# Optimization experiments

Hardware: AMD Instinct MI355X
Metric: run time of the kernel (lower is better)

Reference implementation:

```python
import jax, jax.numpy as jnp
import numpy as np

B, M, D = 16, 16, 512          # m (tokens per sample) must equal num_experts
N = 16                          # num_experts
H = (D + D) * 2 // 3            # hidden_dim = 682
OUT = 512


def setup_inputs() -> dict:
    key = jax.random.key(0)
    ks = jax.random.split(key, 8)
    s = lambda k, shape, fan: jax.random.normal(k, shape, jnp.float32) / np.sqrt(fan)
    return {
        "x":    jax.random.normal(ks[0], (B, M, D), jnp.float32),
        "phi":  jax.random.normal(ks[1], (D, N, H), jnp.float32),
        "W1":   s(ks[2], (N, D, H), D),
        "b1":   s(ks[3], (N, H), D),
        "W2":   s(ks[4], (N, H, D), H),
        "b2":   s(ks[5], (N, D), H),
        "Wout": s(ks[6], (N * D, OUT), N * D),
        "bout": s(ks[7], (OUT,), N * D),
    }


def reference(x, phi, W1, b1, W2, b2, Wout, bout):
    # dispatch/combine logits: [b, m, n, p]
    logits = jnp.einsum('bmd,dnp->bmnp', x, phi)
    Dw = jax.nn.softmax(logits, axis=1)                       # dispatch weights over tokens m
    Cw = jax.nn.softmax(jax.nn.softmax(logits, axis=2), axis=3)  # (softmax of softmax, faithful)
    Xs = jnp.einsum('bmd,bmnp->bnpd', x, Dw)                  # expert slot inputs [b,n,p,d]
    # batched per-expert MLP (grouped GEMM over expert axis n)
    hmid = jax.nn.relu(jnp.einsum('bnpd,ndh->bnph', Xs, W1) + b1[None, :, None, :])
    Ys = jnp.einsum('bnph,nhd->bnpd', hmid, W2) + b2[None, :, None, :]
    Y = jnp.einsum('bnpd,bmnp->bmd', Ys, Cw)                  # combine -> [b, m, d]
    flat = Y.reshape(Y.shape[0], -1)                          # [b, m*d] == [b, n*d]
    return flat @ Wout + bout
```

## Files before the change

kernel.cpp:

```cpp
#include <hip/hip_runtime.h>
#include <hip/hip_bf16.h>
#include <math.h>

typedef unsigned int   u32;
typedef unsigned short u16;
typedef __bf16 bf16;
typedef bf16  bf16x8  __attribute__((ext_vector_type(8)));
typedef float f32x4   __attribute__((ext_vector_type(4)));
typedef float f32x16  __attribute__((ext_vector_type(16)));

#define BBATCH 16
#define MTOK   16
#define NEXP   16
#define DDIM   512
#define HDIM   682
#define HPAD   704
#define NHCOL  (NEXP*HDIM)
#define NHPCOL (NEXP*HPAD)
#define BM     (BBATCH*MTOK)

__device__ __forceinline__ u16 f2bf(float f) {
    u32 u = __builtin_bit_cast(u32, f);
    u += 0x7fffu + ((u >> 16) & 1u);
    return (u16)(u >> 16);
}
__device__ __forceinline__ float bf2f(u16 h) {
    u32 u = ((u32)h) << 16;
    return __builtin_bit_cast(float, u);
}
__device__ __forceinline__ u32 pk2bf(float a, float b) {
    __hip_bfloat162 t = __float22bfloat162_rn(float2{a, b});
    u32 r;
    __builtin_memcpy(&r, &t, 4);
    return r;
}

__global__ __launch_bounds__(256) void k_prep(
    const float* __restrict__ x, const float* __restrict__ b2,
    const float* __restrict__ bout,
    u16* __restrict__ xh, u16* __restrict__ xl,
    float* __restrict__ Y, float* __restrict__ out, u16* __restrict__ DwT) {
    const int bid = blockIdx.x, tid = threadIdx.x;
    if (bid < 128) {
        int i = (bid * 256 + tid) * 4;
        float4 v = *(const float4*)&x[i];
        float a[4] = {v.x, v.y, v.z, v.w};
        u16 hh[4], ll[4];
        #pragma unroll
        for (int j = 0; j < 4; ++j) {
            hh[j] = f2bf(a[j]);
            ll[j] = f2bf(a[j] - bf2f(hh[j]));
        }
        *(uint2*)&xh[i] = make_uint2((u32)hh[0] | ((u32)hh[1] << 16), (u32)hh[2] | ((u32)hh[3] << 16));
        *(uint2*)&xl[i] = make_uint2((u32)ll[0] | ((u32)ll[1] << 16), (u32)ll[2] | ((u32)ll[3] << 16));
    } else if (bid < 640) {
        int idx = (bid - 128) * 256 + tid;
        int d = idx & 511;
        float s = 0.f;
        #pragma unroll
        for (int nn = 0; nn < 16; ++nn) s += b2[nn * 512 + d];
        Y[idx] = s;
    } else if (bid < 672) {
        int idx = (bid - 640) * 256 + tid;
        out[idx] = bout[idx & 511];
    } else {
        int g = (bid - 672) * 256 + tid;
        int bn = g / 88, off = g - bn * 88;
        *(uint2*)(DwT + (size_t)(bn * HPAD + HDIM) * 16 + off * 4) = make_uint2(0u, 0u);
    }
}

__global__ __launch_bounds__(256) void k_lgemm(
    const u16* __restrict__ xh, const u16* __restrict__ xl,
    const float* __restrict__ phi, float* __restrict__ C,
    u16* __restrict__ DwT) {
    __shared__ u16 AH[128 * 40], AL[128 * 40], BH[64 * 40], BL[64 * 40];
    __shared__ float F[32 * 68];
    const int ct = blockIdx.x, rt = blockIdx.y;
    const int tid = threadIdx.x;
    const int wv = tid >> 6, lane = tid & 63, quad = lane >> 4, l15 = lane & 15;
    f32x4 acc[2][4] = {};
    for (int kb = 0; kb < 512; kb += 32) {
        {
            int rr = tid >> 2, kg = (tid & 3) * 8;
            #pragma unroll
            for (int rp = 0; rp < 2; ++rp) {
                int r = rp * 64 + rr;
                size_t ao = (size_t)(rt * 128 + r) * 512 + kb + kg;
                *(uint4*)&AH[r * 40 + kg] = *(const uint4*)(xh + ao);
                *(uint4*)&AL[r * 40 + kg] = *(const uint4*)(xl + ao);
            }
        }
        {
            int dl = tid >> 3, cg = (tid & 7) * 8;
            int c0 = ct * 64 + cg;
            const float* src = phi + (size_t)(kb + dl) * NHCOL + c0;
            float v[8];
            if (c0 + 8 <= NHCOL) {
                *(float4*)&v[0] = *(const float4*)&src[0];
                *(float4*)&v[4] = *(const float4*)&src[4];
            } else {
                #pragma unroll
                for (int i = 0; i < 8; ++i) v[i] = (c0 + i < NHCOL) ? src[i] : 0.f;
            }
            #pragma unroll
            for (int i = 0; i < 8; ++i) F[dl * 68 + cg + i] = v[i];
        }
        __syncthreads();
        {
            int cc = tid & 63, q = tid >> 6;
            u16 th[8], tl[8];
            #pragma unroll
            for (int i = 0; i < 8; ++i) {
                float v = F[(q * 8 + i) * 68 + cc];
                th[i] = f2bf(v);
                tl[i] = f2bf(v - bf2f(th[i]));
            }
            *(uint4*)&BH[cc * 40 + q * 8] = *(uint4*)&th[0];
            *(uint4*)&BL[cc * 40 + q * 8] = *(uint4*)&tl[0];
        }
        __syncthreads();
        bf16x8 ah[2], al[2];
        #pragma unroll
        for (int i = 0; i < 2; ++i) {
            ah[i] = *(const bf16x8*)&AH[(wv * 32 + i * 16 + l15) * 40 + quad * 8];
            al[i] = *(const bf16x8*)&AL[(wv * 32 + i * 16 + l15) * 40 + quad * 8];
        }
        #pragma unroll
        for (int j = 0; j < 4; ++j) {
            bf16x8 bh = *(const bf16x8*)&BH[(j * 16 + l15) * 40 + quad * 8];
            bf16x8 bl = *(const bf16x8*)&BL[(j * 16 + l15) * 40 + quad * 8];
            #pragma unroll
            for (int i = 0; i < 2; ++i) {
                acc[i][j] = __builtin_amdgcn_mfma_f32_16x16x32_bf16(ah[i], bh, acc[i][j], 0, 0, 0);
                acc[i][j] = __builtin_amdgcn_mfma_f32_16x16x32_bf16(ah[i], bl, acc[i][j], 0, 0, 0);
                acc[i][j] = __builtin_amdgcn_mfma_f32_16x16x32_bf16(al[i], bh, acc[i][j], 0, 0, 0);
            }
        }
        __syncthreads();
    }
    #pragma unroll
    for (int i = 0; i < 2; ++i) {
        const int b  = rt * 8 + wv * 2 + i;
        const int r0 = rt * 128 + wv * 32 + i * 16 + quad * 4;
        #pragma unroll
        for (int j = 0; j < 4; ++j) {
            const int col = ct * 64 + j * 16 + l15;
            float a0 = acc[i][j][0], a1 = acc[i][j][1], a2 = acc[i][j][2], a3 = acc[i][j][3];
            if (col < NHCOL) {
                C[(size_t)(r0 + 0) * NHCOL + col] = a0;
                C[(size_t)(r0 + 1) * NHCOL + col] = a1;
                C[(size_t)(r0 + 2) * NHCOL + col] = a2;
                C[(size_t)(r0 + 3) * NHCOL + col] = a3;
            }
            float mx = fmaxf(fmaxf(a0, a1), fmaxf(a2, a3));
            mx = fmaxf(mx, __shfl_xor(mx, 16));
            mx = fmaxf(mx, __shfl_xor(mx, 32));
            float e0 = expf(a0 - mx), e1 = expf(a1 - mx);
            float e2 = expf(a2 - mx), e3 = expf(a3 - mx);
            float s = e0 + e1 + e2 + e3;
            s += __shfl_xor(s, 16);
            s += __shfl_xor(s, 32);
            float inv = 1.f / s;
            if (col < NHCOL) {
                int n = col / HDIM;
                int p = col - n * HDIM;
                u16* dst = DwT + ((size_t)((b * 16 + n) * HPAD + p)) * 16 + quad * 4;
                *(uint2*)dst = make_uint2(pk2bf(e0 * inv, e1 * inv), pk2bf(e2 * inv, e3 * inv));
            }
        }
    }
}

__global__ __launch_bounds__(256) void k_t1cw(
    const u16* __restrict__ A, const float* __restrict__ W1,
    u16* __restrict__ T1b,
    const float* __restrict__ L, u16* __restrict__ CwB) {
    __shared__ __align__(16) char smem[NHCOL * 4];
    const int bid = blockIdx.x, tid = threadIdx.x;
    if (bid < 176) {
        u16*   As = (u16*)smem;
        u16*   Bs = (u16*)(smem + 20480);
        float* F  = (float*)(smem + 25600);
        const int ct = bid;
        const int wv = tid >> 6, lane = tid & 63, quad = lane >> 4, l15 = lane & 15;
        const int n = ct / 11, h0 = (ct % 11) * 64;
        f32x4 acc[4][4] = {};
        for (int kb = 0; kb < 512; kb += 32) {
            {
                int rr = tid >> 2, kg = (tid & 3) * 8;
                #pragma unroll
                for (int rp = 0; rp < 4; ++rp) {
                    int r = rp * 64 + rr;
                    *(uint4*)&As[r * 40 + kg] = *(const uint4*)(A + (size_t)r * 512 + kb + kg);
                }
            }
            {
                int dl = tid >> 3, cg = (tid & 7) * 8;
                int h = h0 + cg;
                const float* wr = W1 + ((size_t)n * 512 + kb + dl) * HDIM + h;
                float v[8];
                if (h + 8 <= HDIM) {
                    #pragma unroll
                    for (int i = 0; i < 4; ++i) {
                        float2 t = *(const float2*)&wr[i * 2];
                        v[i * 2] = t.x; v[i * 2 + 1] = t.y;
                    }
                } else {
                    #pragma unroll
                    for (int i = 0; i < 8; ++i) v[i] = (h + i < HDIM) ? wr[i] : 0.f;
                }
                #pragma unroll
                for (int i = 0; i < 8; ++i) F[dl * 68 + cg + i] = v[i];
            }
            __syncthreads();
            {
                int cc = tid & 63, q = tid >> 6;
                u16 tv[8];
                #pragma unroll
                for (int i = 0; i < 8; ++i) tv[i] = f2bf(F[(q * 8 + i) * 68 + cc]);
                *(uint4*)&Bs[cc * 40 + q * 8] = *(uint4*)&tv[0];
            }
            __syncthreads();
            bf16x8 af[4], bfr[4];
            #pragma unroll
            for (int i = 0; i < 4; ++i)
                af[i] = *(const bf16x8*)&As[(wv * 64 + i * 16 + l15) * 40 + quad * 8];
            #pragma unroll
            for (int j = 0; j < 4; ++j)
                bfr[j] = *(const bf16x8*)&Bs[(j * 16 + l15) * 40 + quad * 8];
            #pragma unroll
            for (int i = 0; i < 4; ++i)
                #pragma unroll
                for (int j = 0; j < 4; ++j)
                    acc[i][j] = __builtin_amdgcn_mfma_f32_16x16x32_bf16(af[i], bfr[j], acc[i][j], 0, 0, 0);
            __syncthreads();
        }
        #pragma unroll
        for (int i = 0; i < 4; ++i)
            #pragma unroll
            for (int j = 0; j < 4; ++j) {
                int col = ct * 64 + j * 16 + l15;
                int r0  = wv * 64 + i * 16 + quad * 4;
                #pragma unroll
                for (int r = 0; r < 4; ++r)
                    T1b[(size_t)(r0 + r) * NHPCOL + col] = f2bf(acc[i][j][r]);
            }
    } else {
        float* row = (float*)smem;
        const int j = bid - 176;
        const int m = j & 15, b = j >> 4;
        const float* Lrow = L + (size_t)(b * 16 + m) * NHCOL;
        for (int i = tid; i < NHCOL; i += 256) row[i] = Lrow[i];
        __syncthreads();
        for (int p = tid; p < HDIM; p += 256) {
            float v[16];
            float mx = -1e30f;
            #pragma unroll
            for (int n = 0; n < 16; ++n) { v[n] = row[n * HDIM + p]; mx = fmaxf(mx, v[n]); }
            float s = 0.f;
            #pragma unroll
            for (int n = 0; n < 16; ++n) { v[n] = expf(v[n] - mx); s += v[n]; }
            float inv = 1.f / s;
            #pragma unroll
            for (int n = 0; n < 16; ++n) row[n * HDIM + p] = expf(v[n] * inv);
        }
        __syncthreads();
        const int wv = tid >> 6, lane = tid & 63;
        for (int nn = 0; nn < 4; ++nn) {
            int n = wv * 4 + nn;
            float s = 0.f;
            for (int p = lane; p < HDIM; p += 64) s += row[n * HDIM + p];
            #pragma unroll
            for (int off = 32; off > 0; off >>= 1) s += __shfl_xor(s, off);
            float inv = 1.f / s;
            u16* dst = CwB + (size_t)(((b * 16 + n) * 16 + m)) * HPAD;
            for (int p = lane; p < HDIM; p += 64) dst[p] = f2bf(row[n * HDIM + p] * inv);
            if (lane < HPAD - HDIM) dst[HDIM + lane] = 0;
        }
    }
}

__global__ __launch_bounds__(256) void k_mid(
    const u16* __restrict__ T1b, const u16* __restrict__ DwT,
    const u16* __restrict__ CwB, const float* __restrict__ b1,
    u16* __restrict__ Gb) {
    __shared__ u16 T1T[128 * 24];
    __shared__ u16 hmidT[128 * 64];
    const int ht = blockIdx.x, n = blockIdx.y, b = blockIdx.z;
    const int tid = threadIdx.x;
    const int wv = tid >> 6, lane = tid & 63;
    const int quad = lane >> 4, l15 = lane & 15;
    const int l31 = lane & 31, half = lane >> 5;
    const int h0 = ht * 128;
    const int b16n = b * 16 + n;

    {
        int m = tid & 15, hh0 = (tid >> 4) * 8;
        u16 v[8];
        if (h0 + hh0 + 8 <= HPAD) {
            *(uint4*)v = *(const uint4*)(T1b + (size_t)(b * 16 + m) * NHPCOL + n * HPAD + h0 + hh0);
        } else {
            #pragma unroll
            for (int i = 0; i < 8; ++i) v[i] = 0;
        }
        #pragma unroll
        for (int i = 0; i < 8; ++i) T1T[(hh0 + i) * 24 + m] = v[i];
    }
    __syncthreads();

    const int hrow = wv * 32 + l31;
    bf16x8 bt1 = *(const bf16x8*)&T1T[hrow * 24 + half * 8];
    int hg1 = h0 + hrow;
    float biasf = (hg1 < HDIM) ? b1[n * HDIM + hg1] : 0.f;
    f32x16 cbias;
    #pragma unroll
    for (int i = 0; i < 16; ++i) cbias[i] = biasf;

    const u16* dwbase = DwT + (size_t)(b16n * HPAD) * 16;
    const u16* cwrow  = CwB + (size_t)(b16n * 16 + l15) * HPAD;

    f32x4 acc[2] = {};
    const int hsw = hrow & 7;
    for (int c = 0; c < 11; ++c) {
        const int p0 = c * 64;
        #pragma unroll
        for (int pt = 0; pt < 2; ++pt) {
            bf16x8 adw = *(const bf16x8*)(dwbase + (size_t)(p0 + pt * 32 + l31) * 16 + half * 8);
            f32x16 hm = __builtin_amdgcn_mfma_f32_32x32x16_bf16(adw, bt1, cbias, 0, 0, 0);
            #pragma unroll
            for (int g = 0; g < 4; ++g) {
                float v0 = fmaxf(hm[g * 4 + 0], 0.f);
                float v1 = fmaxf(hm[g * 4 + 1], 0.f);
                float v2 = fmaxf(hm[g * 4 + 2], 0.f);
                float v3 = fmaxf(hm[g * 4 + 3], 0.f);
                uint2 pk = make_uint2(pk2bf(v0, v1), pk2bf(v2, v3));
                int gran = (pt * 4 + g) ^ hsw;
                *(uint2*)&hmidT[hrow * 64 + gran * 8 + half * 4] = pk;
            }
        }
        #pragma unroll
        for (int s = 0; s < 2; ++s) {
            bf16x8 acw = *(const bf16x8*)(cwrow + p0 + s * 32 + quad * 8);
            #pragma unroll
            for (int hj = 0; hj < 2; ++hj) {
                int hr = wv * 32 + hj * 16 + l15;
                int gr = (s * 4 + quad) ^ (hr & 7);
                bf16x8 bh = *(const bf16x8*)&hmidT[hr * 64 + gr * 8];
                acc[hj] = __builtin_amdgcn_mfma_f32_16x16x32_bf16(acw, bh, acc[hj], 0, 0, 0);
            }
        }
    }
    #pragma unroll
    for (int hj = 0; hj < 2; ++hj) {
        int h = h0 + wv * 32 + hj * 16 + l15;
        if (h < HPAD) {
            #pragma unroll
            for (int r = 0; r < 4; ++r) {
                int m = quad * 4 + r;
                Gb[(size_t)(b * 16 + m) * NHPCOL + n * HPAD + h] = f2bf(acc[hj][r]);
            }
        }
    }
}

__global__ __launch_bounds__(256) void k_ygemm(
    const u16* __restrict__ G, const float* __restrict__ W2, float* __restrict__ Y) {
    __shared__ u16 AsL[64 * 40];
    __shared__ u16 BsL[128 * 40];
    __shared__ float F[32 * 132];
    const int ct = blockIdx.x, rt = blockIdx.y, nz = blockIdx.z;
    const int n = nz >> 1, kb0 = (nz & 1) * 352;
    const int tid = threadIdx.x;
    const int wv = tid >> 6, lane = tid & 63, quad = lane >> 4, l15 = lane & 15;
    const int m0 = rt * 64, d0 = ct * 128;
    f32x4 acc[4][2] = {};
    for (int kb = kb0; kb < kb0 + 352; kb += 32) {
        {
            int am = tid >> 2, akg = (tid & 3) * 8;
            *(uint4*)&AsL[am * 40 + akg] =
                *(const uint4*)(G + (size_t)(m0 + am) * NHPCOL + n * HPAD + kb + akg);
        }
        {
            int hl = tid >> 3, cg = (tid & 7) * 16;
            int h = kb + hl;
            float v[16];
            if (h < HDIM) {
                const float* src = W2 + ((size_t)n * HDIM + h) * 512 + d0 + cg;
                *(float4*)&v[0]  = *(const float4*)&src[0];
                *(float4*)&v[4]  = *(const float4*)&src[4];
                *(float4*)&v[8]  = *(const float4*)&src[8];
                *(float4*)&v[12] = *(const float4*)&src[12];
            } else {
                #pragma unroll
                for (int i = 0; i < 16; ++i) v[i] = 0.f;
            }
            #pragma unroll
            for (int i = 0; i < 16; ++i) F[hl * 132 + cg + i] = v[i];
        }
        __syncthreads();
        {
            int cc = tid & 127, half = tid >> 7;
            u16 tv[16];
            #pragma unroll
            for (int i = 0; i < 16; ++i) tv[i] = f2bf(F[(half * 16 + i) * 132 + cc]);
            *(uint4*)&BsL[cc * 40 + half * 16]     = *(uint4*)&tv[0];
            *(uint4*)&BsL[cc * 40 + half * 16 + 8] = *(uint4*)&tv[8];
        }
        __syncthreads();
        bf16x8 af[4], bfr[2];
        #pragma unroll
        for (int i = 0; i < 4; ++i) af[i] = *(const bf16x8*)&AsL[(i * 16 + l15) * 40 + quad * 8];
        #pragma unroll
        for (int j = 0; j < 2; ++j) bfr[j] = *(const bf16x8*)&BsL[(wv * 32 + j * 16 + l15) * 40 + quad * 8];
        #pragma unroll
        for (int i = 0; i < 4; ++i)
            #pragma unroll
            for (int j = 0; j < 2; ++j)
                acc[i][j] = __builtin_amdgcn_mfma_f32_16x16x32_bf16(af[i], bfr[j], acc[i][j], 0, 0, 0);
        __syncthreads();
    }
    #pragma unroll
    for (int i = 0; i < 4; ++i)
        #pragma unroll
        for (int j = 0; j < 2; ++j) {
            int d = d0 + wv * 32 + j * 16 + l15;
            int r0 = m0 + i * 16 + quad * 4;
            #pragma unroll
            for (int r = 0; r < 4; ++r)
                atomicAdd(&Y[(size_t)(r0 + r) * 512 + d], acc[i][j][r]);
        }
}

__global__ __launch_bounds__(256) void k_outgemm(
    const float* __restrict__ Y, const float* __restrict__ Wout, float* __restrict__ out) {
    __shared__ u16 AsL[16 * 40];
    __shared__ u16 BsL[128 * 40];
    __shared__ float F[32 * 132];
    const int ct = blockIdx.x, ks = blockIdx.y;
    const int tid = threadIdx.x;
    const int wv = tid >> 6, lane = tid & 63, quad = lane >> 4, l15 = lane & 15;
    const int o0 = ct * 128, kbase = ks * 128;
    f32x4 acc[2] = {};
    for (int kb = 0; kb < 128; kb += 32) {
        {
            int r = tid >> 4, k2 = (tid & 15) * 2;
            float2 v = *(const float2*)&Y[(size_t)r * 8192 + kbase + kb + k2];
            AsL[r * 40 + k2]     = f2bf(v.x);
            AsL[r * 40 + k2 + 1] = f2bf(v.y);
        }
        {
            int kl = tid >> 3, cg = (tid & 7) * 16;
            const float* src = Wout + (size_t)(kbase + kb + kl) * 512 + o0 + cg;
            float v[16];
            *(float4*)&v[0]  = *(const float4*)&src[0];
            *(float4*)&v[4]  = *(const float4*)&src[4];
            *(float4*)&v[8]  = *(const float4*)&src[8];
            *(float4*)&v[12] = *(const float4*)&src[12];
            #pragma unroll
            for (int i = 0; i < 16; ++i) F[kl * 132 + cg + i] = v[i];
        }
        __syncthreads();
        {
            int cc = tid & 127, half = tid >> 7;
            u16 tv[16];
            #pragma unroll
            for (int i = 0; i < 16; ++i) tv[i] = f2bf(F[(half * 16 + i) * 132 + cc]);
            *(uint4*)&BsL[cc * 40 + half * 16]     = *(uint4*)&tv[0];
            *(uint4*)&BsL[cc * 40 + half * 16 + 8] = *(uint4*)&tv[8];
        }
        __syncthreads();
        bf16x8 af = *(const bf16x8*)&AsL[l15 * 40 + quad * 8];
        #pragma unroll
        for (int j = 0; j < 2; ++j) {
            bf16x8 bfr = *(const bf16x8*)&BsL[(wv * 32 + j * 16 + l15) * 40 + quad * 8];
            acc[j] = __builtin_amdgcn_mfma_f32_16x16x32_bf16(af, bfr, acc[j], 0, 0, 0);
        }
        __syncthreads();
    }
    #pragma unroll
    for (int j = 0; j < 2; ++j) {
        int o = o0 + wv * 32 + j * 16 + l15;
        #pragma unroll
        for (int r = 0; r < 4; ++r)
            atomicAdd(&out[(size_t)(quad * 4 + r) * 512 + o], acc[j][r]);
    }
}

extern "C" void kernel_launch(void* const* d_in, const int* in_sizes, int n_in,
                              void* d_out, int out_size, void* d_ws, size_t ws_size,
                              hipStream_t stream) {
    const float* x    = (const float*)d_in[0];
    const float* phi  = (const float*)d_in[1];
    const float* W1   = (const float*)d_in[2];
    const float* b1   = (const float*)d_in[3];
    const float* W2   = (const float*)d_in[4];
    const float* b2   = (const float*)d_in[5];
    const float* Wout = (const float*)d_in[6];
    const float* bout = (const float*)d_in[7];
    float* out = (float*)d_out;

    char* base = (char*)d_ws;
    float* logits = (float*)(base + 0);
    u16*   DwT    = (u16*)(base + 11173888);
    u16*   CwB    = (u16*)(base + 16941056);
    u16*   T1b    = (u16*)(base + 22708224);
    u16*   Gb     = (u16*)(base + 28475392);
    u16*   xh     = (u16*)(base + 34242560);
    u16*   xl     = (u16*)(base + 34504704);
    float* Y      = (float*)(base + 34766848);

    k_prep    <<<dim3(760), 256, 0, stream>>>(x, b2, bout, xh, xl, Y, out, DwT);
    k_lgemm   <<<dim3(171, 2), 256, 0, stream>>>(xh, xl, phi, logits, DwT);
    k_t1cw    <<<dim3(432), 256, 0, stream>>>(xh, W1, T1b, logits, CwB);
    k_mid     <<<dim3(6, 16, 16), 256, 0, stream>>>(T1b, DwT, CwB, b1, Gb);
    k_ygemm   <<<dim3(4, 4, 32), 256, 0, stream>>>(Gb, W2, Y);
    k_outgemm <<<dim3(4, 64), 256, 0, stream>>>(Y, Wout, out);
}
```

Measured before the change: 233.9 us.

## Pre-transpose weights to bf16 in prep kernel and prefetch GEMM tiles via registers

```diff
diff --git a/kernel.cpp b/kernel.cpp
--- a/kernel.cpp
+++ b/kernel.cpp
@@ -17,7 +17,7 @@
 #define HPAD   704
 #define NHCOL  (NEXP*HDIM)
 #define NHPCOL (NEXP*HPAD)
-#define BM     (BBATCH*MTOK)
+#define PHIROWS 10944
 
 __device__ __forceinline__ u16 f2bf(float f) {
     u32 u = __builtin_bit_cast(u32, f);
@@ -35,11 +35,69 @@
     return r;
 }
 
+__device__ __forceinline__ void tr_tile(
+    const float* __restrict__ in, int inStride, int validR, int validC,
+    int r0, int c0, u16* __restrict__ outH, u16* __restrict__ outL,
+    int outStride, bool split, int tid, u16* TL) {
+    u16* Lh = TL;
+    u16* Ll = TL + 64 * 72;
+    const int lr = tid >> 2, cb = (tid & 3) * 16;
+    u16 hv[16], lv[16];
+    #pragma unroll
+    for (int i = 0; i < 16; ++i) { hv[i] = 0; lv[i] = 0; }
+    const int r = r0 + lr;
+    if (r < validR) {
+        const float* src = in + (size_t)r * inStride + c0 + cb;
+        #pragma unroll
+        for (int i = 0; i < 16; i += 2) {
+            int c = c0 + cb + i;
+            float a0 = 0.f, a1 = 0.f;
+            if (c + 2 <= validC) { float2 t = *(const float2*)&src[i]; a0 = t.x; a1 = t.y; }
+            else {
+                if (c < validC)     a0 = src[i];
+                if (c + 1 < validC) a1 = src[i + 1];
+            }
+            hv[i]     = f2bf(a0);
+            hv[i + 1] = f2bf(a1);
+            if (split) {
+                lv[i]     = f2bf(a0 - bf2f(hv[i]));
+                lv[i + 1] = f2bf(a1 - bf2f(hv[i + 1]));
+            }
+        }
+    }
+    #pragma unroll
+    for (int i = 0; i < 16; ++i) Lh[lr * 72 + cb + i] = hv[i];
+    if (split) {
+        #pragma unroll
+        for (int i = 0; i < 16; ++i) Ll[lr * 72 + cb + i] = lv[i];
+    }
+    __syncthreads();
+    const int oc = tid >> 2, rj = (tid & 3) * 16;
+    u16 ov[16];
+    #pragma unroll
+    for (int i = 0; i < 16; ++i) ov[i] = Lh[(rj + i) * 72 + oc];
+    u16* dst = outH + (size_t)(c0 + oc) * outStride + r0 + rj;
+    *(uint4*)dst       = *(uint4*)&ov[0];
+    *(uint4*)(dst + 8) = *(uint4*)&ov[8];
+    if (split) {
+        #pragma unroll
+        for (int i = 0; i < 16; ++i) ov[i] = Ll[(rj + i) * 72 + oc];
+        u16* dstl = outL + (size_t)(c0 + oc) * outStride + r0 + rj;
+        *(uint4*)dstl       = *(uint4*)&ov[0];
+        *(uint4*)(dstl + 8) = *(uint4*)&ov[8];
+    }
+}
+
 __global__ __launch_bounds__(256) void k_prep(
     const float* __restrict__ x, const float* __restrict__ b2,
     const float* __restrict__ bout,
+    const float* __restrict__ phi, const float* __restrict__ W1,
+    const float* __restrict__ W2, const float* __restrict__ Wout,
     u16* __restrict__ xh, u16* __restrict__ xl,
-    float* __restrict__ Y, float* __restrict__ out, u16* __restrict__ DwT) {
+    float* __restrict__ Y, float* __restrict__ out, u16* __restrict__ DwT,
+    u16* __restrict__ phiTh, u16* __restrict__ phiTl,
+    u16* __restrict__ W1T, u16* __restrict__ W2T, u16* __restrict__ WoutT) {
+    __shared__ u16 TL[2 * 64 * 72];
     const int bid = blockIdx.x, tid = threadIdx.x;
     if (bid < 128) {
         int i = (bid * 256 + tid) * 4;
@@ -63,78 +121,93 @@
     } else if (bid < 672) {
         int idx = (bid - 640) * 256 + tid;
         out[idx] = bout[idx & 511];
-    } else {
+    } else if (bid < 760) {
         int g = (bid - 672) * 256 + tid;
         int bn = g / 88, off = g - bn * 88;
         *(uint2*)(DwT + (size_t)(bn * HPAD + HDIM) * 16 + off * 4) = make_uint2(0u, 0u);
+    } else if (bid < 2128) {
+        int t = bid - 760; int dt = t / 171, ctile = t - dt * 171;
+        tr_tile(phi, NHCOL, 512, NHCOL, dt * 64, ctile * 64,
+                phiTh, phiTl, 512, true, tid, TL);
+    } else if (bid < 3536) {
+        int t = bid - 2128; int n = t / 88, rem = t - n * 88;
+        int dt = rem / 11, ht = rem - dt * 11;
+        tr_tile(W1 + (size_t)n * 512 * HDIM, HDIM, 512, HDIM, dt * 64, ht * 64,
+                W1T + (size_t)n * HPAD * 512, nullptr, 512, false, tid, TL);
+    } else if (bid < 4944) {
+        int t = bid - 3536; int n = t / 88, rem = t - n * 88;
+        int ht = rem / 8, dt = rem - ht * 8;
+        tr_tile(W2 + (size_t)n * HDIM * 512, 512, HDIM, 512, ht * 64, dt * 64,
+                W2T + (size_t)n * 512 * HPAD, nullptr, HPAD, false, tid, TL);
+    } else {
+        int t = bid - 4944; int kt = t >> 3, ot = t & 7;
+        tr_tile(Wout, 512, 8192, 512, kt * 64, ot * 64,
+                WoutT, nullptr, 8192, false, tid, TL);
     }
 }
 
 __global__ __launch_bounds__(256) void k_lgemm(
     const u16* __restrict__ xh, const u16* __restrict__ xl,
-    const float* __restrict__ phi, float* __restrict__ C,
-    u16* __restrict__ DwT) {
-    __shared__ u16 AH[128 * 40], AL[128 * 40], BH[64 * 40], BL[64 * 40];
-    __shared__ float F[32 * 68];
+    const u16* __restrict__ phiTh, const u16* __restrict__ phiTl,
+    float* __restrict__ C, u16* __restrict__ DwT) {
+    __shared__ u16 AH[128 * 72], AL[128 * 72], BH[64 * 72], BL[64 * 72];
     const int ct = blockIdx.x, rt = blockIdx.y;
     const int tid = threadIdx.x;
     const int wv = tid >> 6, lane = tid & 63, quad = lane >> 4, l15 = lane & 15;
+    const int ar = tid >> 1, ac = (tid & 1) * 32;
+    const int br = tid >> 2, bc = (tid & 3) * 16;
+    const u16* aph = xh + (size_t)(rt * 128 + ar) * 512 + ac;
+    const u16* apl = xl + (size_t)(rt * 128 + ar) * 512 + ac;
+    const u16* bph = phiTh + (size_t)(ct * 64 + br) * 512 + bc;
+    const u16* bpl = phiTl + (size_t)(ct * 64 + br) * 512 + bc;
+    uint4 rah[4], ral[4], rbh[2], rbl[2];
+    #pragma unroll
+    for (int i = 0; i < 4; ++i) { rah[i] = *(const uint4*)(aph + i * 8); ral[i] = *(const uint4*)(apl + i * 8); }
+    #pragma unroll
+    for (int j = 0; j < 2; ++j) { rbh[j] = *(const uint4*)(bph + j * 8); rbl[j] = *(const uint4*)(bpl + j * 8); }
     f32x4 acc[2][4] = {};
-    for (int kb = 0; kb < 512; kb += 32) {
-        {
-            int rr = tid >> 2, kg = (tid & 3) * 8;
-            #pragma unroll
-            for (int rp = 0; rp < 2; ++rp) {
-                int r = rp * 64 + rr;
-                size_t ao = (size_t)(rt * 128 + r) * 512 + kb + kg;
-                *(uint4*)&AH[r * 40 + kg] = *(const uint4*)(xh + ao);
-                *(uint4*)&AL[r * 40 + kg] = *(const uint4*)(xl + ao);
-            }
-        }
-        {
-            int dl = tid >> 3, cg = (tid & 7) * 8;
-            int c0 = ct * 64 + cg;
-            const float* src = phi + (size_t)(kb + dl) * NHCOL + c0;
-            float v[8];
-            if (c0 + 8 <= NHCOL) {
-                *(float4*)&v[0] = *(const float4*)&src[0];
-                *(float4*)&v[4] = *(const float4*)&src[4];
-            } else {
+    for (int kb = 0; kb < 512; kb += 64) {
+        #pragma unroll
+        for (int i = 0; i < 4; ++i) {
+            *(uint4*)&AH[ar * 72 + ac + i * 8] = rah[i];
+            *(uint4*)&AL[ar * 72 + ac + i * 8] = ral[i];
+        }
+        #pragma unroll
+        for (int j = 0; j < 2; ++j) {
+            *(uint4*)&BH[br * 72 + bc + j * 8] = rbh[j];
+            *(uint4*)&BL[br * 72 + bc + j * 8] = rbl[j];
+        }
+        __syncthreads();
+        if (kb + 64 < 512) {
+            #pragma unroll
+            for (int i = 0; i < 4; ++i) {
+                rah[i] = *(const uint4*)(aph + kb + 64 + i * 8);
+                ral[i] = *(const uint4*)(apl + kb + 64 + i * 8);
+            }
+            #pragma unroll
+            for (int j = 0; j < 2; ++j) {
+                rbh[j] = *(const uint4*)(bph + kb + 64 + j * 8);
+                rbl[j] = *(const uint4*)(bpl + kb + 64 + j * 8);
+            }
+        }
+        #pragma unroll
+        for (int ks = 0; ks < 2; ++ks) {
+            bf16x8 ah[2], al[2];
+            #pragma unroll
+            for (int i = 0; i < 2; ++i) {
+                ah[i] = *(const bf16x8*)&AH[(wv * 32 + i * 16 + l15) * 72 + ks * 32 + quad * 8];
+                al[i] = *(const bf16x8*)&AL[(wv * 32 + i * 16 + l15) * 72 + ks * 32 + quad * 8];
+            }
+            #pragma unroll
+            for (int j = 0; j < 4; ++j) {
+                bf16x8 bh = *(const bf16x8*)&BH[(j * 16 + l15) * 72 + ks * 32 + quad * 8];
+                bf16x8 bl = *(const bf16x8*)&BL[(j * 16 + l15) * 72 + ks * 32 + quad * 8];
                 #pragma unroll
-                for (int i = 0; i < 8; ++i) v[i] = (c0 + i < NHCOL) ? src[i] : 0.f;
-            }
-            #pragma unroll
-            for (int i = 0; i < 8; ++i) F[dl * 68 + cg + i] = v[i];
-        }
-        __syncthreads();
-        {
-            int cc = tid & 63, q = tid >> 6;
-            u16 th[8], tl[8];
-            #pragma unroll
-            for (int i = 0; i < 8; ++i) {
-                float v = F[(q * 8 + i) * 68 + cc];
-                th[i] = f2bf(v);
-                tl[i] = f2bf(v - bf2f(th[i]));
-            }
-            *(uint4*)&BH[cc * 40 + q * 8] = *(uint4*)&th[0];
-            *(uint4*)&BL[cc * 40 + q * 8] = *(uint4*)&tl[0];
-        }
-        __syncthreads();
-        bf16x8 ah[2], al[2];
-        #pragma unroll
-        for (int i = 0; i < 2; ++i) {
-            ah[i] = *(const bf16x8*)&AH[(wv * 32 + i * 16 + l15) * 40 + quad * 8];
-            al[i] = *(const bf16x8*)&AL[(wv * 32 + i * 16 + l15) * 40 + quad * 8];
-        }
-        #pragma unroll
-        for (int j = 0; j < 4; ++j) {
-            bf16x8 bh = *(const bf16x8*)&BH[(j * 16 + l15) * 40 + quad * 8];
-            bf16x8 bl = *(const bf16x8*)&BL[(j * 16 + l15) * 40 + quad * 8];
-            #pragma unroll
-            for (int i = 0; i < 2; ++i) {
-                acc[i][j] = __builtin_amdgcn_mfma_f32_16x16x32_bf16(ah[i], bh, acc[i][j], 0, 0, 0);
-                acc[i][j] = __builtin_amdgcn_mfma_f32_16x16x32_bf16(ah[i], bl, acc[i][j], 0, 0, 0);
-                acc[i][j] = __builtin_amdgcn_mfma_f32_16x16x32_bf16(al[i], bh, acc[i][j], 0, 0, 0);
+                for (int i = 0; i < 2; ++i) {
+                    acc[i][j] = __builtin_amdgcn_mfma_f32_16x16x32_bf16(ah[i], bh, acc[i][j], 0, 0, 0);
+                    acc[i][j] = __builtin_amdgcn_mfma_f32_16x16x32_bf16(ah[i], bl, acc[i][j], 0, 0, 0);
+                    acc[i][j] = __builtin_amdgcn_mfma_f32_16x16x32_bf16(al[i], bh, acc[i][j], 0, 0, 0);
+                }
             }
         }
         __syncthreads();
@@ -173,55 +246,35 @@
 }
 
 __global__ __launch_bounds__(256) void k_t1cw(
-    const u16* __restrict__ A, const float* __restrict__ W1,
+    const u16* __restrict__ A, const u16* __restrict__ W1T,
     u16* __restrict__ T1b,
     const float* __restrict__ L, u16* __restrict__ CwB) {
     __shared__ __align__(16) char smem[NHCOL * 4];
     const int bid = blockIdx.x, tid = threadIdx.x;
     if (bid < 176) {
-        u16*   As = (u16*)smem;
-        u16*   Bs = (u16*)(smem + 20480);
-        float* F  = (float*)(smem + 25600);
+        u16* As = (u16*)smem;
+        u16* Bs = (u16*)(smem + 20480);
         const int ct = bid;
         const int wv = tid >> 6, lane = tid & 63, quad = lane >> 4, l15 = lane & 15;
         const int n = ct / 11, h0 = (ct % 11) * 64;
+        const u16* ap = A + (size_t)tid * 512;
+        const int br = tid >> 2, bc = (tid & 3) * 8;
+        const u16* bp = W1T + ((size_t)n * HPAD + h0 + br) * 512 + bc;
+        uint4 ra[4], rb;
+        #pragma unroll
+        for (int i = 0; i < 4; ++i) ra[i] = *(const uint4*)(ap + i * 8);
+        rb = *(const uint4*)bp;
         f32x4 acc[4][4] = {};
         for (int kb = 0; kb < 512; kb += 32) {
-            {
-                int rr = tid >> 2, kg = (tid & 3) * 8;
+            #pragma unroll
+            for (int i = 0; i < 4; ++i) *(uint4*)&As[tid * 40 + i * 8] = ra[i];
+            *(uint4*)&Bs[br * 40 + bc] = rb;
+            __syncthreads();
+            if (kb + 32 < 512) {
                 #pragma unroll
-                for (int rp = 0; rp < 4; ++rp) {
-                    int r = rp * 64 + rr;
-                    *(uint4*)&As[r * 40 + kg] = *(const uint4*)(A + (size_t)r * 512 + kb + kg);
-                }
-            }
-            {
-                int dl = tid >> 3, cg = (tid & 7) * 8;
-                int h = h0 + cg;
-                const float* wr = W1 + ((size_t)n * 512 + kb + dl) * HDIM + h;
-                float v[8];
-                if (h + 8 <= HDIM) {
-                    #pragma unroll
-                    for (int i = 0; i < 4; ++i) {
-                        float2 t = *(const float2*)&wr[i * 2];
-                        v[i * 2] = t.x; v[i * 2 + 1] = t.y;
-                    }
-                } else {
-                    #pragma unroll
-                    for (int i = 0; i < 8; ++i) v[i] = (h + i < HDIM) ? wr[i] : 0.f;
-                }
-                #pragma unroll
-                for (int i = 0; i < 8; ++i) F[dl * 68 + cg + i] = v[i];
-            }
-            __syncthreads();
-            {
-                int cc = tid & 63, q = tid >> 6;
-                u16 tv[8];
-                #pragma unroll
-                for (int i = 0; i < 8; ++i) tv[i] = f2bf(F[(q * 8 + i) * 68 + cc]);
-                *(uint4*)&Bs[cc * 40 + q * 8] = *(uint4*)&tv[0];
-            }
-            __syncthreads();
+                for (int i = 0; i < 4; ++i) ra[i] = *(const uint4*)(ap + kb + 32 + i * 8);
+                rb = *(const uint4*)(bp + kb + 32);
+            }
             bf16x8 af[4], bfr[4];
             #pragma unroll
             for (int i = 0; i < 4; ++i)
@@ -365,54 +418,36 @@
 }
 
 __global__ __launch_bounds__(256) void k_ygemm(
-    const u16* __restrict__ G, const float* __restrict__ W2, float* __restrict__ Y) {
-    __shared__ u16 AsL[64 * 40];
-    __shared__ u16 BsL[128 * 40];
-    __shared__ float F[32 * 132];
+    const u16* __restrict__ G, const u16* __restrict__ W2T, float* __restrict__ Y) {
+    __shared__ u16 As[64 * 40], Bs[128 * 40];
     const int ct = blockIdx.x, rt = blockIdx.y, nz = blockIdx.z;
     const int n = nz >> 1, kb0 = (nz & 1) * 352;
     const int tid = threadIdx.x;
     const int wv = tid >> 6, lane = tid & 63, quad = lane >> 4, l15 = lane & 15;
     const int m0 = rt * 64, d0 = ct * 128;
+    const int am = tid >> 2, ak = (tid & 3) * 8;
+    const int bd = tid >> 1, bk = (tid & 1) * 16;
+    const u16* apg = G + (size_t)(m0 + am) * NHPCOL + n * HPAD + ak;
+    const u16* bpg = W2T + ((size_t)n * 512 + d0 + bd) * HPAD + bk;
+    uint4 ra  = *(const uint4*)(apg + kb0);
+    uint4 rb0 = *(const uint4*)(bpg + kb0);
+    uint4 rb1 = *(const uint4*)(bpg + kb0 + 8);
     f32x4 acc[4][2] = {};
     for (int kb = kb0; kb < kb0 + 352; kb += 32) {
-        {
-            int am = tid >> 2, akg = (tid & 3) * 8;
-            *(uint4*)&AsL[am * 40 + akg] =
-                *(const uint4*)(G + (size_t)(m0 + am) * NHPCOL + n * HPAD + kb + akg);
-        }
-        {
-            int hl = tid >> 3, cg = (tid & 7) * 16;
-            int h = kb + hl;
-            float v[16];
-            if (h < HDIM) {
-                const float* src = W2 + ((size_t)n * HDIM + h) * 512 + d0 + cg;
-                *(float4*)&v[0]  = *(const float4*)&src[0];
-                *(float4*)&v[4]  = *(const float4*)&src[4];
-                *(float4*)&v[8]  = *(const float4*)&src[8];
-                *(float4*)&v[12] = *(const float4*)&src[12];
-            } else {
-                #pragma unroll
-                for (int i = 0; i < 16; ++i) v[i] = 0.f;
-            }
-            #pragma unroll
-            for (int i = 0; i < 16; ++i) F[hl * 132 + cg + i] = v[i];
-        }
-        __syncthreads();
-        {
-            int cc = tid & 127, half = tid >> 7;
-            u16 tv[16];
-            #pragma unroll
-            for (int i = 0; i < 16; ++i) tv[i] = f2bf(F[(half * 16 + i) * 132 + cc]);
-            *(uint4*)&BsL[cc * 40 + half * 16]     = *(uint4*)&tv[0];
-            *(uint4*)&BsL[cc * 40 + half * 16 + 8] = *(uint4*)&tv[8];
-        }
-        __syncthreads();
+        *(uint4*)&As[am * 40 + ak] = ra;
+        *(uint4*)&Bs[bd * 40 + bk] = rb0;
+        *(uint4*)&Bs[bd * 40 + bk + 8] = rb1;
+        __syncthreads();
+        if (kb + 32 < kb0 + 352) {
+            ra  = *(const uint4*)(apg + kb + 32);
+            rb0 = *(const uint4*)(bpg + kb + 32);
+            rb1 = *(const uint4*)(bpg + kb + 40);
+        }
         bf16x8 af[4], bfr[2];
         #pragma unroll
-        for (int i = 0; i < 4; ++i) af[i] = *(const bf16x8*)&AsL[(i * 16 + l15) * 40 + quad * 8];
-        #pragma unroll
-        for (int j = 0; j < 2; ++j) bfr[j] = *(const bf16x8*)&BsL[(wv * 32 + j * 16 + l15) * 40 + quad * 8];
+        for (int i = 0; i < 4; ++i) af[i] = *(const bf16x8*)&As[(i * 16 + l15) * 40 + quad * 8];
+        #pragma unroll
+        for (int j = 0; j < 2; ++j) bfr[j] = *(const bf16x8*)&Bs[(wv * 32 + j * 16 + l15) * 40 + quad * 8];
         #pragma unroll
         for (int i = 0; i < 4; ++i)
             #pragma unroll
@@ -433,47 +468,35 @@
 }
 
 __global__ __launch_bounds__(256) void k_outgemm(
-    const float* __restrict__ Y, const float* __restrict__ Wout, float* __restrict__ out) {
-    __shared__ u16 AsL[16 * 40];
-    __shared__ u16 BsL[128 * 40];
-    __shared__ float F[32 * 132];
+    const float* __restrict__ Y, const u16* __restrict__ WoutT, float* __restrict__ out) {
+    __shared__ u16 As[16 * 40], Bs[128 * 40];
     const int ct = blockIdx.x, ks = blockIdx.y;
     const int tid = threadIdx.x;
     const int wv = tid >> 6, lane = tid & 63, quad = lane >> 4, l15 = lane & 15;
     const int o0 = ct * 128, kbase = ks * 128;
+    const int r_ = tid >> 4, k2 = (tid & 15) * 2;
+    const int bo = tid >> 1, bk = (tid & 1) * 16;
+    const float* ypg = Y + (size_t)r_ * 8192 + kbase + k2;
+    const u16* bpg = WoutT + (size_t)(o0 + bo) * 8192 + kbase + bk;
+    float2 ya = *(const float2*)ypg;
+    uint4 rb0 = *(const uint4*)bpg;
+    uint4 rb1 = *(const uint4*)(bpg + 8);
     f32x4 acc[2] = {};
     for (int kb = 0; kb < 128; kb += 32) {
-        {
-            int r = tid >> 4, k2 = (tid & 15) * 2;
-            float2 v = *(const float2*)&Y[(size_t)r * 8192 + kbase + kb + k2];
-            AsL[r * 40 + k2]     = f2bf(v.x);
-            AsL[r * 40 + k2 + 1] = f2bf(v.y);
-        }
-        {
-            int kl = tid >> 3, cg = (tid & 7) * 16;
-            const float* src = Wout + (size_t)(kbase + kb + kl) * 512 + o0 + cg;
-            float v[16];
-            *(float4*)&v[0]  = *(const float4*)&src[0];
-            *(float4*)&v[4]  = *(const float4*)&src[4];
-            *(float4*)&v[8]  = *(const float4*)&src[8];
-            *(float4*)&v[12] = *(const float4*)&src[12];
-            #pragma unroll
-            for (int i = 0; i < 16; ++i) F[kl * 132 + cg + i] = v[i];
-        }
-        __syncthreads();
-        {
-            int cc = tid & 127, half = tid >> 7;
-            u16 tv[16];
-            #pragma unroll
-            for (int i = 0; i < 16; ++i) tv[i] = f2bf(F[(half * 16 + i) * 132 + cc]);
-            *(uint4*)&BsL[cc * 40 + half * 16]     = *(uint4*)&tv[0];
-            *(uint4*)&BsL[cc * 40 + half * 16 + 8] = *(uint4*)&tv[8];
-        }
-        __syncthreads();
-        bf16x8 af = *(const bf16x8*)&AsL[l15 * 40 + quad * 8];
+        As[r_ * 40 + k2]     = f2bf(ya.x);
+        As[r_ * 40 + k2 + 1] = f2bf(ya.y);
+        *(uint4*)&Bs[bo * 40 + bk]     = rb0;
+        *(uint4*)&Bs[bo * 40 + bk + 8] = rb1;
+        __syncthreads();
+        if (kb + 32 < 128) {
+            ya  = *(const float2*)(ypg + kb + 32);
+            rb0 = *(const uint4*)(bpg + kb + 32);
+            rb1 = *(const uint4*)(bpg + kb + 40);
+        }
+        bf16x8 af = *(const bf16x8*)&As[l15 * 40 + quad * 8];
         #pragma unroll
         for (int j = 0; j < 2; ++j) {
-            bf16x8 bfr = *(const bf16x8*)&BsL[(wv * 32 + j * 16 + l15) * 40 + quad * 8];
+            bf16x8 bfr = *(const bf16x8*)&Bs[(wv * 32 + j * 16 + l15) * 40 + quad * 8];
             acc[j] = __builtin_amdgcn_mfma_f32_16x16x32_bf16(af, bfr, acc[j], 0, 0, 0);
         }
         __syncthreads();
@@ -509,11 +532,18 @@
     u16*   xh     = (u16*)(base + 34242560);
     u16*   xl     = (u16*)(base + 34504704);
     float* Y      = (float*)(base + 34766848);
-
-    k_prep    <<<dim3(760), 256, 0, stream>>>(x, b2, bout, xh, xl, Y, out, DwT);
-    k_lgemm   <<<dim3(171, 2), 256, 0, stream>>>(xh, xl, phi, logits, DwT);
-    k_t1cw    <<<dim3(432), 256, 0, stream>>>(xh, W1, T1b, logits, CwB);
+    u16*   phiTh  = (u16*)(base + 35291136);
+    u16*   phiTl  = (u16*)(base + 46497792);
+    u16*   W1T    = (u16*)(base + 57704448);
+    u16*   W2T    = (u16*)(base + 69238784);
+    u16*   WoutT  = (u16*)(base + 80773120);
+
+    k_prep    <<<dim3(5968), 256, 0, stream>>>(x, b2, bout, phi, W1, W2, Wout,
+                                               xh, xl, Y, out, DwT,
+                                               phiTh, phiTl, W1T, W2T, WoutT);
+    k_lgemm   <<<dim3(171, 2), 256, 0, stream>>>(xh, xl, phiTh, phiTl, logits, DwT);
+    k_t1cw    <<<dim3(432), 256, 0, stream>>>(xh, W1T, T1b, logits, CwB);
     k_mid     <<<dim3(6, 16, 16), 256, 0, stream>>>(T1b, DwT, CwB, b1, Gb);
-    k_ygemm   <<<dim3(4, 4, 32), 256, 0, stream>>>(Gb, W2, Y);
-    k_outgemm <<<dim3(4, 64), 256, 0, stream>>>(Y, Wout, out);
-}
+    k_ygemm   <<<dim3(4, 4, 32), 256, 0, stream>>>(Gb, W2T, Y);
+    k_outgemm <<<dim3(4, 64), 256, 0, stream>>>(Y, WoutT, out);
+}
```

After: 290.8 us. 1.24x slower.
